# Performance work log

Measured on AMD Instinct MI355X. Metric: run time of the kernel, lower is better.

Reference implementation:

```python
import jax, jax.numpy as jnp
import numpy as np

N_EMBD = 1024
N_HEAD = 16
HEAD_DIM = 64


def setup_inputs() -> dict:
    key = jax.random.key(0)
    ks = jax.random.split(key, 5)
    x = jax.random.normal(ks[0], (4, 2048, N_EMBD), dtype=jnp.float32)
    # qkv_proj: Linear(n_embd, 3*n_embd) -- torch weight is [out, in]
    W_qkv = jax.random.normal(ks[1], (3 * N_EMBD, N_EMBD), dtype=jnp.float32) * 0.02
    b_qkv = jnp.zeros((3 * N_EMBD,), dtype=jnp.float32)
    W_out = jax.random.normal(ks[2], (N_EMBD, N_EMBD), dtype=jnp.float32) * 0.02
    b_out = jnp.zeros((N_EMBD,), dtype=jnp.float32)
    return {"x": x, "W_qkv": W_qkv, "b_qkv": b_qkv, "W_out": W_out, "b_out": b_out}


def reference(x, W_qkv, b_qkv, W_out, b_out):
    B, S, C = x.shape
    scale = 1.0 / np.sqrt(HEAD_DIM)
    qkv = jnp.einsum('bsc,oc->bso', x, W_qkv) + b_qkv  # [B,S,3C]
    q, k, v = jnp.split(qkv, 3, axis=-1)
    # [B,S,C] -> [B,H,S,Dh]
    def to_heads(t):
        return t.reshape(B, S, N_HEAD, HEAD_DIM).transpose(0, 2, 1, 3)
    q, k, v = to_heads(q), to_heads(k), to_heads(v)
    scores = jnp.einsum('bhqd,bhkd->bhqk', q, k) * scale  # [B,H,S,S]
    causal = jnp.tril(jnp.ones((S, S), dtype=bool))
    scores = jnp.where(causal[None, None], scores, -jnp.inf)
    weights = jax.nn.softmax(scores.astype(jnp.float32), axis=-1).astype(q.dtype)
    y = jnp.einsum('bhqk,bhkd->bhqd', weights, v)  # [B,H,S,Dh]
    y = y.transpose(0, 2, 1, 3).reshape(B, S, C)
    return jnp.einsum('bsc,oc->bso', y, W_out) + b_out
```

## Files before the change

### kernel.cpp

```cpp
#include <hip/hip_runtime.h>
#include <stdint.h>
#include <stddef.h>

typedef __attribute__((ext_vector_type(8))) short short8;
typedef __attribute__((ext_vector_type(4))) float f32x4;
typedef __attribute__((ext_vector_type(16))) float f32x16;
typedef __attribute__((ext_vector_type(4))) unsigned short ushort4v;

#define SEQ   2048
#define NH    16
#define BATCH 4
#define GK    1024

__device__ __forceinline__ unsigned short f2bf(float f) {
  union { float f; unsigned int u; } v; v.f = f;
  unsigned int u = v.u;
  u += 0x7fffu + ((u >> 16) & 1u);
  return (unsigned short)(u >> 16);
}

__global__ void cvt_bf16(const float* __restrict__ src, unsigned short* __restrict__ dst, int n4) {
  int i = blockIdx.x * blockDim.x + threadIdx.x;
  const int stride = gridDim.x * blockDim.x;
  for (; i < n4; i += stride) {
    const float4 v = reinterpret_cast<const float4*>(src)[i];
    ushort4v o;
    o[0] = f2bf(v.x); o[1] = f2bf(v.y); o[2] = f2bf(v.z); o[3] = f2bf(v.w);
    reinterpret_cast<ushort4v*>(dst)[i] = o;
  }
}

template<int MODE>
__global__ __launch_bounds__(256, 2)
void gemm_bt(const unsigned short* __restrict__ A,
             const unsigned short* __restrict__ Bw,
             const float* __restrict__ bias,
             unsigned short* __restrict__ q_ws,
             unsigned short* __restrict__ k_ws,
             unsigned short* __restrict__ vt_ws,
             float* __restrict__ fout,
             int N)
{
  __shared__ __attribute__((aligned(16))) unsigned short As[128 * 64];
  __shared__ __attribute__((aligned(16))) unsigned short Bs[128 * 64];

  const int t = threadIdx.x;
  const int w = t >> 6, lane = t & 63;
  const int g = lane >> 4, c = lane & 15;
  const int wrow = w >> 1, wcol = w & 1;
  const int m0 = blockIdx.y * 128;
  const int n0 = blockIdx.x * 128;

  const f32x4 fz = {0.f, 0.f, 0.f, 0.f};
  f32x4 acc[4][4];
#pragma unroll
  for (int i = 0; i < 4; ++i)
#pragma unroll
    for (int j = 0; j < 4; ++j) acc[i][j] = fz;

  int s_row[4], s_cg[4], s_off[4];
#pragma unroll
  for (int i = 0; i < 4; ++i) {
    const int u = (i * 4 + w) * 64 + lane;
    s_row[i] = u >> 3;
    s_cg[i]  = u & 7;
    s_off[i] = s_row[i] * 64 + ((s_cg[i] ^ (s_row[i] & 7)) << 3);
  }

  short8 ra[4], rb[4];
#pragma unroll
  for (int i = 0; i < 4; ++i) {
    ra[i] = *reinterpret_cast<const short8*>(A  + (size_t)(m0 + s_row[i]) * GK + s_cg[i] * 8);
    rb[i] = *reinterpret_cast<const short8*>(Bw + (size_t)(n0 + s_row[i]) * GK + s_cg[i] * 8);
  }

  for (int ks = 0; ks < GK; ks += 64) {
#pragma unroll
    for (int i = 0; i < 4; ++i) {
      *reinterpret_cast<short8*>(&As[s_off[i]]) = ra[i];
      *reinterpret_cast<short8*>(&Bs[s_off[i]]) = rb[i];
    }
    __syncthreads();
    const bool more = (ks + 64) < GK;
    if (more) {
#pragma unroll
      for (int i = 0; i < 4; ++i) {
        ra[i] = *reinterpret_cast<const short8*>(A  + (size_t)(m0 + s_row[i]) * GK + (ks + 64) + s_cg[i] * 8);
        rb[i] = *reinterpret_cast<const short8*>(Bw + (size_t)(n0 + s_row[i]) * GK + (ks + 64) + s_cg[i] * 8);
      }
    }
#pragma unroll
    for (int kk = 0; kk < 2; ++kk) {
      short8 af[4], bfr[4];
#pragma unroll
      for (int mi = 0; mi < 4; ++mi) {
        const int row = wrow * 64 + mi * 16 + c;
        af[mi] = *reinterpret_cast<const short8*>(&As[row * 64 + (((kk * 4 + g) ^ (row & 7)) << 3)]);
      }
#pragma unroll
      for (int ni = 0; ni < 4; ++ni) {
        const int row = wcol * 64 + ni * 16 + c;
        bfr[ni] = *reinterpret_cast<const short8*>(&Bs[row * 64 + (((kk * 4 + g) ^ (row & 7)) << 3)]);
      }
#pragma unroll
      for (int mi = 0; mi < 4; ++mi)
#pragma unroll
        for (int ni = 0; ni < 4; ++ni)
          acc[mi][ni] = __builtin_amdgcn_mfma_f32_16x16x32_bf16(af[mi], bfr[ni], acc[mi][ni], 0, 0, 0);
    }
    __syncthreads();
  }

  if (MODE == 0) {
    const int sec = n0 >> 10;
    if (sec == 2) {
#pragma unroll
      for (int ni = 0; ni < 4; ++ni) {
        const int n = n0 + wcol * 64 + ni * 16 + c;
        const float bb = bias[n];
        const int hh = (n & 1023) >> 6;
        const int d = n & 63;
#pragma unroll
        for (int mi = 0; mi < 4; ++mi) {
#pragma unroll
          for (int r = 0; r < 4; ++r) {
            const int m = m0 + wrow * 64 + mi * 16 + g * 4 + r;
            const int b = m >> 11, s = m & 2047;
            vt_ws[((size_t)((b * NH + hh) * 64 + d)) * SEQ + s] = f2bf(acc[mi][ni][r] + bb);
          }
        }
      }
    } else {
      unsigned short* dst = (sec == 0) ? q_ws : k_ws;
      const float qsc = (sec == 0) ? (0.125f * 1.44269504f) : 1.0f;
#pragma unroll
      for (int ni = 0; ni < 4; ++ni) {
        const int n = n0 + wcol * 64 + ni * 16 + c;
        const float bb = bias[n];
        const int hh = (n & 1023) >> 6;
        const int d = n & 63;
#pragma unroll
        for (int mi = 0; mi < 4; ++mi) {
#pragma unroll
          for (int r = 0; r < 4; ++r) {
            const int m = m0 + wrow * 64 + mi * 16 + g * 4 + r;
            const int b = m >> 11, s = m & 2047;
            const float val = (acc[mi][ni][r] + bb) * qsc;
            dst[((size_t)((b * NH + hh) * SEQ + s) << 6) + d] = f2bf(val);
          }
        }
      }
    }
  } else {
#pragma unroll
    for (int ni = 0; ni < 4; ++ni) {
      const int n = n0 + wcol * 64 + ni * 16 + c;
      const float bb = bias[n];
#pragma unroll
      for (int mi = 0; mi < 4; ++mi) {
#pragma unroll
        for (int r = 0; r < 4; ++r) {
          const int m = m0 + wrow * 64 + mi * 16 + g * 4 + r;
          fout[(size_t)m * N + n] = acc[mi][ni][r] + bb;
        }
      }
    }
  }
}

__global__ __launch_bounds__(256, 2)
void attn_fwd2(const unsigned short* __restrict__ q_ws,
               const unsigned short* __restrict__ k_ws,
               const unsigned short* __restrict__ vt_ws,
               unsigned short* __restrict__ y_ws)
{
  __shared__ __attribute__((aligned(16))) unsigned short Ks[2][64 * 64];
  __shared__ __attribute__((aligned(16))) unsigned short Vs[2][64 * 64];
  __shared__ __attribute__((aligned(16))) unsigned short Pl[4][32 * 64];

  const int t = threadIdx.x;
  const int w = t >> 6, lane = t & 63;
  const int ql = lane & 31;
  const int hi = lane >> 5;
  const int bh = blockIdx.y;
  const int b = bh >> 4, h = bh & 15;

  const int s_row = t >> 3, s_cg = t & 7;
  const int s_off0 = s_row * 64 + ((s_cg ^ (s_row & 7)) << 3);
  const int s_off1 = (s_row + 32) * 64 + ((s_cg ^ (s_row & 7)) << 3);

  unsigned short* Pw = &Pl[w][0];

  short8 rk0, rk1, rv0, rv1;
  const unsigned short* kbase = k_ws + (size_t)bh * SEQ * 64;
  const unsigned short* vbase = vt_ws + (size_t)bh * 64 * SEQ;

  auto stage_issue = [&](int kt) {
    const unsigned short* kp = kbase + (size_t)kt * 64 * 64;
    rk0 = *reinterpret_cast<const short8*>(kp + (size_t)s_row * 64 + s_cg * 8);
    rk1 = *reinterpret_cast<const short8*>(kp + (size_t)(s_row + 32) * 64 + s_cg * 8);
    const unsigned short* vp = vbase + (size_t)kt * 64;
    rv0 = *reinterpret_cast<const short8*>(vp + (size_t)s_row * SEQ + s_cg * 8);
    rv1 = *reinterpret_cast<const short8*>(vp + (size_t)(s_row + 32) * SEQ + s_cg * 8);
  };
  auto stage_write = [&](int bi) {
    *reinterpret_cast<short8*>(&Ks[bi][s_off0]) = rk0;
    *reinterpret_cast<short8*>(&Ks[bi][s_off1]) = rk1;
    *reinterpret_cast<short8*>(&Vs[bi][s_off0]) = rv0;
    *reinterpret_cast<short8*>(&Vs[bi][s_off1]) = rv1;
  };

#pragma unroll 1
  for (int pi = 0; pi < 2; ++pi) {
    const int jt = pi ? (15 - blockIdx.x) : blockIdx.x;
    const int q0 = jt * 128;
    const int wq0 = q0 + w * 32;
    const int nkt = 2 * jt + 2;

    const unsigned short* qrow = q_ws + ((size_t)bh * SEQ + (wq0 + ql)) * 64;
    short8 qf[4];
#pragma unroll
    for (int ks = 0; ks < 4; ++ks)
      qf[ks] = *reinterpret_cast<const short8*>(qrow + ks * 16 + hi * 8);

    f32x16 o0, o1;
#pragma unroll
    for (int i = 0; i < 16; ++i) { o0[i] = 0.f; o1[i] = 0.f; }
    float m_run = -1e30f, lsum = 0.f;

    stage_issue(0);
    stage_write(0);

#pragma unroll 1
    for (int kt = 0; kt < nkt; ++kt) {
      const bool more = (kt + 1) < nkt;
      if (more) stage_issue(kt + 1);
      __syncthreads();
      const int cur = kt & 1;
      const int kt64 = kt * 64;

      if (kt64 <= wq0 + 31) {
        f32x16 sc0, sc1;
#pragma unroll
        for (int i = 0; i < 16; ++i) { sc0[i] = 0.f; sc1[i] = 0.f; }
#pragma unroll
        for (int ks = 0; ks < 4; ++ks) {
          const int r0 = ql, r1 = 32 + ql;
          const short8 kf0 = *reinterpret_cast<const short8*>(
              &Ks[cur][r0 * 64 + (((2 * ks + hi) ^ (r0 & 7)) << 3)]);
          const short8 kf1 = *reinterpret_cast<const short8*>(
              &Ks[cur][r1 * 64 + (((2 * ks + hi) ^ (r1 & 7)) << 3)]);
          sc0 = __builtin_amdgcn_mfma_f32_32x32x16_bf16(kf0, qf[ks], sc0, 0, 0, 0);
          sc1 = __builtin_amdgcn_mfma_f32_32x32x16_bf16(kf1, qf[ks], sc1, 0, 0, 0);
        }
        if (kt64 + 63 > wq0) {
          const int gq = wq0 + ql;
#pragma unroll
          for (int r = 0; r < 16; ++r) {
            const int krow = (r & 3) + 8 * (r >> 2) + 4 * hi;
            if (kt64 + krow > gq)      sc0[r] = -1e30f;
            if (kt64 + 32 + krow > gq) sc1[r] = -1e30f;
          }
        }
        float tm = -1e30f;
#pragma unroll
        for (int r = 0; r < 16; ++r) tm = fmaxf(tm, fmaxf(sc0[r], sc1[r]));
        tm = fmaxf(tm, __shfl_xor(tm, 32));
        if (__any(tm > m_run + 10.0f)) {
          const float m_new = fmaxf(m_run, tm);
          const float al = __builtin_amdgcn_exp2f(m_run - m_new);
          m_run = m_new;
          lsum *= al;
#pragma unroll
          for (int r = 0; r < 16; ++r) {
            const int qq = (r & 3) + 8 * (r >> 2) + 4 * hi;
            const float ar = __shfl(al, qq);
            o0[r] *= ar; o1[r] *= ar;
          }
        }
        float psum = 0.f;
#pragma unroll
        for (int t2 = 0; t2 < 2; ++t2) {
#pragma unroll
          for (int gr = 0; gr < 4; ++gr) {
            const float s0 = (t2 ? sc1[gr * 4 + 0] : sc0[gr * 4 + 0]) - m_run;
            const float s1 = (t2 ? sc1[gr * 4 + 1] : sc0[gr * 4 + 1]) - m_run;
            const float s2 = (t2 ? sc1[gr * 4 + 2] : sc0[gr * 4 + 2]) - m_run;
            const float s3 = (t2 ? sc1[gr * 4 + 3] : sc0[gr * 4 + 3]) - m_run;
            const float p0 = __builtin_amdgcn_exp2f(s0);
            const float p1 = __builtin_amdgcn_exp2f(s1);
            const float p2 = __builtin_amdgcn_exp2f(s2);
            const float p3 = __builtin_amdgcn_exp2f(s3);
            psum += (p0 + p1) + (p2 + p3);
            uint2 pv;
            pv.x = (unsigned)f2bf(p0) | ((unsigned)f2bf(p1) << 16);
            pv.y = (unsigned)f2bf(p2) | ((unsigned)f2bf(p3) << 16);
            const int off = ql * 64 + (((gr + 4 * t2) ^ (ql & 7)) << 3) + 4 * hi;
            *reinterpret_cast<uint2*>(&Pw[off]) = pv;
          }
        }
        lsum += psum;
        short8 pa[4];
#pragma unroll
        for (int ks = 0; ks < 4; ++ks)
          pa[ks] = *reinterpret_cast<const short8*>(
              &Pw[ql * 64 + (((2 * ks + hi) ^ (ql & 7)) << 3)]);
#pragma unroll
        for (int ks = 0; ks < 4; ++ks) {
          const int r0 = ql, r1 = 32 + ql;
          const short8 vf0 = *reinterpret_cast<const short8*>(
              &Vs[cur][r0 * 64 + (((2 * ks + hi) ^ (r0 & 7)) << 3)]);
          const short8 vf1 = *reinterpret_cast<const short8*>(
              &Vs[cur][r1 * 64 + (((2 * ks + hi) ^ (r1 & 7)) << 3)]);
          o0 = __builtin_amdgcn_mfma_f32_32x32x16_bf16(pa[ks], vf0, o0, 0, 0, 0);
          o1 = __builtin_amdgcn_mfma_f32_32x32x16_bf16(pa[ks], vf1, o1, 0, 0, 0);
        }
      }
      if (more) stage_write((kt + 1) & 1);
    }

    lsum += __shfl_xor(lsum, 32);
    const float linv = 1.f / lsum;
#pragma unroll
    for (int r = 0; r < 16; ++r) {
      const int qq = (r & 3) + 8 * (r >> 2) + 4 * hi;
      const float lr = __shfl(linv, qq);
      const size_t rowo = ((size_t)b * SEQ + (wq0 + qq)) * 1024 + h * 64;
      y_ws[rowo + ql]      = f2bf(o0[r] * lr);
      y_ws[rowo + 32 + ql] = f2bf(o1[r] * lr);
    }
    __syncthreads();
  }
}

extern "C" void kernel_launch(void* const* d_in, const int* in_sizes, int n_in,
                              void* d_out, int out_size, void* d_ws, size_t ws_size,
                              hipStream_t stream)
{
  (void)in_sizes; (void)n_in; (void)out_size; (void)ws_size;
  const float* x     = (const float*)d_in[0];
  const float* W_qkv = (const float*)d_in[1];
  const float* b_qkv = (const float*)d_in[2];
  const float* W_out = (const float*)d_in[3];
  const float* b_out = (const float*)d_in[4];
  float* out = (float*)d_out;

  unsigned short* ws      = (unsigned short*)d_ws;
  unsigned short* x_bf    = ws;
  unsigned short* wqkv_bf = x_bf    + (size_t)8192 * 1024;
  unsigned short* wout_bf = wqkv_bf + (size_t)3072 * 1024;
  unsigned short* q_ws    = wout_bf + (size_t)1024 * 1024;
  unsigned short* k_ws    = q_ws    + (size_t)64 * SEQ * 64;
  unsigned short* vt_ws   = k_ws    + (size_t)64 * SEQ * 64;
  unsigned short* y_ws    = vt_ws   + (size_t)64 * SEQ * 64;

  cvt_bf16<<<2048, 256, 0, stream>>>(x,     x_bf,    (8192 * 1024) / 4);
  cvt_bf16<<<1024, 256, 0, stream>>>(W_qkv, wqkv_bf, (3072 * 1024) / 4);
  cvt_bf16<<<512,  256, 0, stream>>>(W_out, wout_bf, (1024 * 1024) / 4);

  gemm_bt<0><<<dim3(24, 64), 256, 0, stream>>>(x_bf, wqkv_bf, b_qkv, q_ws, k_ws, vt_ws, nullptr, 3072);
  attn_fwd2<<<dim3(8, 64), 256, 0, stream>>>(q_ws, k_ws, vt_ws, y_ws);
  gemm_bt<1><<<dim3(8, 64), 256, 0, stream>>>(y_ws, wout_bf, b_out, nullptr, nullptr, nullptr, out, 1024);
}
```

Measured before the change: 185.0 us.

## Rework GEMM loads to direct-to-LDS, separate V transpose, larger attention query tiles

The GEMM now stages A/B tiles through global_load_lds directly into shared memory instead of register prefetch, dropping the software double-buffering. The V output of the QKV GEMM is written row-major and then transposed by a separate kernel, replacing the strided scattered stores. The attention kernel now processes 64 query rows per wave (two 32-row subtiles sharing K/V fragments). P is packed into MFMA operands in registers via cvt_pk_bf16 and permlane32 swaps instead of round-tripping through LDS. This trades an extra kernel launch and the loss of GEMM prefetch overlap for better K/V reuse and less LDS traffic. It also halves the attention grid, which may reduce occupancy.

```diff
diff --git a/kernel.cpp b/kernel.cpp
--- a/kernel.cpp
+++ b/kernel.cpp
@@ -6,6 +6,7 @@
 typedef __attribute__((ext_vector_type(4))) float f32x4;
 typedef __attribute__((ext_vector_type(16))) float f32x16;
 typedef __attribute__((ext_vector_type(4))) unsigned short ushort4v;
+typedef __attribute__((ext_vector_type(4))) unsigned int uint4v;
 
 #define SEQ   2048
 #define NH    16
@@ -17,6 +18,32 @@
   unsigned int u = v.u;
   u += 0x7fffu + ((u >> 16) & 1u);
   return (unsigned short)(u >> 16);
+}
+
+__device__ __forceinline__ unsigned cvtpk_bf16(float lo, float hi) {
+  unsigned r;
+  asm("v_cvt_pk_bf16_f32 %0, %1, %2" : "=v"(r) : "v"(lo), "v"(hi));
+  return r;
+}
+
+__device__ __forceinline__ void plswap(unsigned &x, unsigned &y) {
+#if __has_builtin(__builtin_amdgcn_permlane32_swap)
+  auto r = __builtin_amdgcn_permlane32_swap((int)x, (int)y, false, false);
+  x = (unsigned)r[0]; y = (unsigned)r[1];
+#else
+  const unsigned sx = (unsigned)__shfl_xor((int)x, 32);
+  const unsigned sy = (unsigned)__shfl_xor((int)y, 32);
+  const bool hi = (threadIdx.x & 63) >= 32;
+  const unsigned nx = hi ? sy : x;
+  const unsigned ny = hi ? y : sx;
+  x = nx; y = ny;
+#endif
+}
+
+__device__ __forceinline__ void gload16(const unsigned short* g, unsigned short* l) {
+  __builtin_amdgcn_global_load_lds(
+      (const __attribute__((address_space(1))) unsigned int*)g,
+      (__attribute__((address_space(3))) unsigned int*)l, 16, 0, 0);
 }
 
 __global__ void cvt_bf16(const float* __restrict__ src, unsigned short* __restrict__ dst, int n4) {
@@ -37,7 +64,7 @@
              const float* __restrict__ bias,
              unsigned short* __restrict__ q_ws,
              unsigned short* __restrict__ k_ws,
-             unsigned short* __restrict__ vt_ws,
+             unsigned short* __restrict__ v_ws,
              float* __restrict__ fout,
              int N)
 {
@@ -51,6 +78,9 @@
   const int m0 = blockIdx.y * 128;
   const int n0 = blockIdx.x * 128;
 
+  const int r8 = lane >> 3;
+  const int cgs = (lane & 7) ^ r8;
+
   const f32x4 fz = {0.f, 0.f, 0.f, 0.f};
   f32x4 acc[4][4];
 #pragma unroll
@@ -58,37 +88,15 @@
 #pragma unroll
     for (int j = 0; j < 4; ++j) acc[i][j] = fz;
 
-  int s_row[4], s_cg[4], s_off[4];
-#pragma unroll
-  for (int i = 0; i < 4; ++i) {
-    const int u = (i * 4 + w) * 64 + lane;
-    s_row[i] = u >> 3;
-    s_cg[i]  = u & 7;
-    s_off[i] = s_row[i] * 64 + ((s_cg[i] ^ (s_row[i] & 7)) << 3);
-  }
-
-  short8 ra[4], rb[4];
-#pragma unroll
-  for (int i = 0; i < 4; ++i) {
-    ra[i] = *reinterpret_cast<const short8*>(A  + (size_t)(m0 + s_row[i]) * GK + s_cg[i] * 8);
-    rb[i] = *reinterpret_cast<const short8*>(Bw + (size_t)(n0 + s_row[i]) * GK + s_cg[i] * 8);
-  }
-
   for (int ks = 0; ks < GK; ks += 64) {
+    __syncthreads();
 #pragma unroll
     for (int i = 0; i < 4; ++i) {
-      *reinterpret_cast<short8*>(&As[s_off[i]]) = ra[i];
-      *reinterpret_cast<short8*>(&Bs[s_off[i]]) = rb[i];
+      const int RB = (i * 4 + w) * 8;
+      gload16(A + (size_t)(m0 + RB + r8) * GK + ks + cgs * 8, &As[RB * 64]);
+      gload16(Bw + (size_t)(n0 + RB + r8) * GK + ks + cgs * 8, &Bs[RB * 64]);
     }
     __syncthreads();
-    const bool more = (ks + 64) < GK;
-    if (more) {
-#pragma unroll
-      for (int i = 0; i < 4; ++i) {
-        ra[i] = *reinterpret_cast<const short8*>(A  + (size_t)(m0 + s_row[i]) * GK + (ks + 64) + s_cg[i] * 8);
-        rb[i] = *reinterpret_cast<const short8*>(Bw + (size_t)(n0 + s_row[i]) * GK + (ks + 64) + s_cg[i] * 8);
-      }
-    }
 #pragma unroll
     for (int kk = 0; kk < 2; ++kk) {
       short8 af[4], bfr[4];
@@ -108,54 +116,34 @@
         for (int ni = 0; ni < 4; ++ni)
           acc[mi][ni] = __builtin_amdgcn_mfma_f32_16x16x32_bf16(af[mi], bfr[ni], acc[mi][ni], 0, 0, 0);
     }
-    __syncthreads();
   }
 
   if (MODE == 0) {
     const int sec = n0 >> 10;
-    if (sec == 2) {
-#pragma unroll
-      for (int ni = 0; ni < 4; ++ni) {
-        const int n = n0 + wcol * 64 + ni * 16 + c;
-        const float bb = bias[n];
-        const int hh = (n & 1023) >> 6;
-        const int d = n & 63;
-#pragma unroll
-        for (int mi = 0; mi < 4; ++mi) {
-#pragma unroll
-          for (int r = 0; r < 4; ++r) {
-            const int m = m0 + wrow * 64 + mi * 16 + g * 4 + r;
-            const int b = m >> 11, s = m & 2047;
-            vt_ws[((size_t)((b * NH + hh) * 64 + d)) * SEQ + s] = f2bf(acc[mi][ni][r] + bb);
-          }
-        }
-      }
-    } else {
-      unsigned short* dst = (sec == 0) ? q_ws : k_ws;
-      const float qsc = (sec == 0) ? (0.125f * 1.44269504f) : 1.0f;
-#pragma unroll
-      for (int ni = 0; ni < 4; ++ni) {
-        const int n = n0 + wcol * 64 + ni * 16 + c;
-        const float bb = bias[n];
-        const int hh = (n & 1023) >> 6;
-        const int d = n & 63;
-#pragma unroll
-        for (int mi = 0; mi < 4; ++mi) {
-#pragma unroll
-          for (int r = 0; r < 4; ++r) {
-            const int m = m0 + wrow * 64 + mi * 16 + g * 4 + r;
-            const int b = m >> 11, s = m & 2047;
-            const float val = (acc[mi][ni][r] + bb) * qsc;
-            dst[((size_t)((b * NH + hh) * SEQ + s) << 6) + d] = f2bf(val);
-          }
-        }
-      }
-    }
-  } else {
+    unsigned short* dst = (sec == 0) ? q_ws : ((sec == 1) ? k_ws : v_ws);
+    const float qsc = (sec == 0) ? (0.125f * 1.44269504f) : 1.0f;
 #pragma unroll
     for (int ni = 0; ni < 4; ++ni) {
       const int n = n0 + wcol * 64 + ni * 16 + c;
       const float bb = bias[n];
+      const int hh = (n & 1023) >> 6;
+      const int d = n & 63;
+#pragma unroll
+      for (int mi = 0; mi < 4; ++mi) {
+#pragma unroll
+        for (int r = 0; r < 4; ++r) {
+          const int m = m0 + wrow * 64 + mi * 16 + g * 4 + r;
+          const int b = m >> 11, s = m & 2047;
+          const float val = (acc[mi][ni][r] + bb) * qsc;
+          dst[((size_t)((b * NH + hh) * SEQ + s) << 6) + d] = f2bf(val);
+        }
+      }
+    }
+  } else {
+#pragma unroll
+    for (int ni = 0; ni < 4; ++ni) {
+      const int n = n0 + wcol * 64 + ni * 16 + c;
+      const float bb = bias[n];
 #pragma unroll
       for (int mi = 0; mi < 4; ++mi) {
 #pragma unroll
@@ -168,68 +156,140 @@
   }
 }
 
+__global__ __launch_bounds__(256)
+void transpose_v(const unsigned short* __restrict__ v, unsigned short* __restrict__ vt) {
+  __shared__ unsigned short T[64][72];
+  const int t = threadIdx.x;
+  const int bh = blockIdx.y, s0 = blockIdx.x * 64;
+  const unsigned short* src = v + ((size_t)bh * SEQ + s0) * 64;
+#pragma unroll
+  for (int rep = 0; rep < 2; ++rep) {
+    const int u = rep * 256 + t;
+    const int sr = u >> 3, cg = u & 7;
+    const short8 x = *reinterpret_cast<const short8*>(src + (size_t)sr * 64 + cg * 8);
+    *reinterpret_cast<short8*>(&T[sr][cg * 8]) = x;
+  }
+  __syncthreads();
+  unsigned short* dst = vt + (size_t)bh * 64 * SEQ + s0;
+#pragma unroll
+  for (int rep = 0; rep < 2; ++rep) {
+    const int u = rep * 256 + t;
+    const int d = u >> 3, sc8 = u & 7;
+    short8 x;
+#pragma unroll
+    for (int j = 0; j < 8; ++j) x[j] = (short)T[sc8 * 8 + j][d];
+    *reinterpret_cast<short8*>(dst + (size_t)d * SEQ + sc8 * 8) = x;
+  }
+}
+
 __global__ __launch_bounds__(256, 2)
-void attn_fwd2(const unsigned short* __restrict__ q_ws,
+void attn_fwd3(const unsigned short* __restrict__ q_ws,
                const unsigned short* __restrict__ k_ws,
                const unsigned short* __restrict__ vt_ws,
                unsigned short* __restrict__ y_ws)
 {
   __shared__ __attribute__((aligned(16))) unsigned short Ks[2][64 * 64];
   __shared__ __attribute__((aligned(16))) unsigned short Vs[2][64 * 64];
-  __shared__ __attribute__((aligned(16))) unsigned short Pl[4][32 * 64];
 
   const int t = threadIdx.x;
   const int w = t >> 6, lane = t & 63;
-  const int ql = lane & 31;
-  const int hi = lane >> 5;
-  const int bh = blockIdx.y;
-  const int b = bh >> 4, h = bh & 15;
+  const int ql = lane & 31, hi = lane >> 5;
+  const int bh = blockIdx.y, b = bh >> 4, h = bh & 15;
 
   const int s_row = t >> 3, s_cg = t & 7;
-  const int s_off0 = s_row * 64 + ((s_cg ^ (s_row & 7)) << 3);
-  const int s_off1 = (s_row + 32) * 64 + ((s_cg ^ (s_row & 7)) << 3);
-
-  unsigned short* Pw = &Pl[w][0];
-
-  short8 rk0, rk1, rv0, rv1;
+  const int so0 = s_row * 64 + ((s_cg ^ (s_row & 7)) << 3);
+  const int so1 = (s_row + 32) * 64 + ((s_cg ^ (s_row & 7)) << 3);
+
   const unsigned short* kbase = k_ws + (size_t)bh * SEQ * 64;
   const unsigned short* vbase = vt_ws + (size_t)bh * 64 * SEQ;
 
+  short8 rk0, rk1, rv0, rv1;
   auto stage_issue = [&](int kt) {
     const unsigned short* kp = kbase + (size_t)kt * 64 * 64;
     rk0 = *reinterpret_cast<const short8*>(kp + (size_t)s_row * 64 + s_cg * 8);
     rk1 = *reinterpret_cast<const short8*>(kp + (size_t)(s_row + 32) * 64 + s_cg * 8);
-    const unsigned short* vp = vbase + (size_t)kt * 64;
+    const unsigned short* vp = vbase + kt * 64;
     rv0 = *reinterpret_cast<const short8*>(vp + (size_t)s_row * SEQ + s_cg * 8);
     rv1 = *reinterpret_cast<const short8*>(vp + (size_t)(s_row + 32) * SEQ + s_cg * 8);
   };
   auto stage_write = [&](int bi) {
-    *reinterpret_cast<short8*>(&Ks[bi][s_off0]) = rk0;
-    *reinterpret_cast<short8*>(&Ks[bi][s_off1]) = rk1;
-    *reinterpret_cast<short8*>(&Vs[bi][s_off0]) = rv0;
-    *reinterpret_cast<short8*>(&Vs[bi][s_off1]) = rv1;
+    *reinterpret_cast<short8*>(&Ks[bi][so0]) = rk0;
+    *reinterpret_cast<short8*>(&Ks[bi][so1]) = rk1;
+    *reinterpret_cast<short8*>(&Vs[bi][so0]) = rv0;
+    *reinterpret_cast<short8*>(&Vs[bi][so1]) = rv1;
   };
 
 #pragma unroll 1
   for (int pi = 0; pi < 2; ++pi) {
-    const int jt = pi ? (15 - blockIdx.x) : blockIdx.x;
-    const int q0 = jt * 128;
-    const int wq0 = q0 + w * 32;
-    const int nkt = 2 * jt + 2;
-
-    const unsigned short* qrow = q_ws + ((size_t)bh * SEQ + (wq0 + ql)) * 64;
-    short8 qf[4];
-#pragma unroll
-    for (int ks = 0; ks < 4; ++ks)
-      qf[ks] = *reinterpret_cast<const short8*>(qrow + ks * 16 + hi * 8);
-
-    f32x16 o0, o1;
-#pragma unroll
-    for (int i = 0; i < 16; ++i) { o0[i] = 0.f; o1[i] = 0.f; }
-    float m_run = -1e30f, lsum = 0.f;
+    const int jt = pi ? (7 - blockIdx.x) : blockIdx.x;
+    const int wq0 = jt * 256 + w * 64;
+    const int nkt = 4 * jt + 4;
+
+    const unsigned short* qrA = q_ws + ((size_t)bh * SEQ + (wq0 + ql)) * 64;
+    const unsigned short* qrB = qrA + 32 * 64;
+    short8 qfA[4], qfB[4];
+#pragma unroll
+    for (int ks = 0; ks < 4; ++ks) {
+      qfA[ks] = *reinterpret_cast<const short8*>(qrA + ks * 16 + hi * 8);
+      qfB[ks] = *reinterpret_cast<const short8*>(qrB + ks * 16 + hi * 8);
+    }
+
+    f32x16 oA0, oA1, oB0, oB1;
+#pragma unroll
+    for (int i = 0; i < 16; ++i) { oA0[i] = 0.f; oA1[i] = 0.f; oB0[i] = 0.f; oB1[i] = 0.f; }
+    float mA = -1e30f, lA = 0.f, mB = -1e30f, lB = 0.f;
 
     stage_issue(0);
     stage_write(0);
+
+    auto softmax_pack = [&](f32x16& s0, f32x16& s1, float& m_run, float& lsum,
+                            f32x16& o0, f32x16& o1, short8* pa) {
+      float tm = -1e30f;
+#pragma unroll
+      for (int r = 0; r < 16; ++r) tm = fmaxf(tm, fmaxf(s0[r], s1[r]));
+      tm = fmaxf(tm, __shfl_xor(tm, 32));
+      if (__any(tm > m_run + 10.0f)) {
+        const float m_new = fmaxf(m_run, tm);
+        const float al = __builtin_amdgcn_exp2f(m_run - m_new);
+        m_run = m_new;
+        lsum *= al;
+#pragma unroll
+        for (int r = 0; r < 16; ++r) {
+          const int qq = (r & 3) + 8 * (r >> 2) + 4 * hi;
+          const float ar = __shfl(al, qq);
+          o0[r] *= ar; o1[r] *= ar;
+        }
+      }
+      float psum = 0.f;
+      unsigned W[16];
+#pragma unroll
+      for (int half = 0; half < 2; ++half) {
+#pragma unroll
+        for (int gr = 0; gr < 4; ++gr) {
+          const float v0 = (half ? s1[gr * 4 + 0] : s0[gr * 4 + 0]) - m_run;
+          const float v1 = (half ? s1[gr * 4 + 1] : s0[gr * 4 + 1]) - m_run;
+          const float v2 = (half ? s1[gr * 4 + 2] : s0[gr * 4 + 2]) - m_run;
+          const float v3 = (half ? s1[gr * 4 + 3] : s0[gr * 4 + 3]) - m_run;
+          const float p0 = __builtin_amdgcn_exp2f(v0);
+          const float p1 = __builtin_amdgcn_exp2f(v1);
+          const float p2 = __builtin_amdgcn_exp2f(v2);
+          const float p3 = __builtin_amdgcn_exp2f(v3);
+          psum += (p0 + p1) + (p2 + p3);
+          W[half * 8 + 2 * gr]     = cvtpk_bf16(p0, p1);
+          W[half * 8 + 2 * gr + 1] = cvtpk_bf16(p2, p3);
+        }
+      }
+      lsum += psum;
+#pragma unroll
+      for (int q4 = 0; q4 < 4; ++q4) {
+        unsigned a0 = W[q4 * 4 + 0], a1 = W[q4 * 4 + 2];
+        unsigned b0 = W[q4 * 4 + 1], b1 = W[q4 * 4 + 3];
+        plswap(a0, a1);
+        plswap(b0, b1);
+        uint4v pk; pk[0] = a0; pk[1] = b0; pk[2] = a1; pk[3] = b1;
+        pa[q4] = __builtin_bit_cast(short8, pk);
+      }
+    };
 
 #pragma unroll 1
     for (int kt = 0; kt < nkt; ++kt) {
@@ -239,96 +299,89 @@
       const int cur = kt & 1;
       const int kt64 = kt * 64;
 
-      if (kt64 <= wq0 + 31) {
-        f32x16 sc0, sc1;
-#pragma unroll
-        for (int i = 0; i < 16; ++i) { sc0[i] = 0.f; sc1[i] = 0.f; }
+      if (kt64 <= wq0 + 63) {
+        short8 kfl[4], kfh[4];
 #pragma unroll
         for (int ks = 0; ks < 4; ++ks) {
-          const int r0 = ql, r1 = 32 + ql;
-          const short8 kf0 = *reinterpret_cast<const short8*>(
-              &Ks[cur][r0 * 64 + (((2 * ks + hi) ^ (r0 & 7)) << 3)]);
-          const short8 kf1 = *reinterpret_cast<const short8*>(
-              &Ks[cur][r1 * 64 + (((2 * ks + hi) ^ (r1 & 7)) << 3)]);
-          sc0 = __builtin_amdgcn_mfma_f32_32x32x16_bf16(kf0, qf[ks], sc0, 0, 0, 0);
-          sc1 = __builtin_amdgcn_mfma_f32_32x32x16_bf16(kf1, qf[ks], sc1, 0, 0, 0);
-        }
-        if (kt64 + 63 > wq0) {
-          const int gq = wq0 + ql;
-#pragma unroll
-          for (int r = 0; r < 16; ++r) {
-            const int krow = (r & 3) + 8 * (r >> 2) + 4 * hi;
-            if (kt64 + krow > gq)      sc0[r] = -1e30f;
-            if (kt64 + 32 + krow > gq) sc1[r] = -1e30f;
+          kfl[ks] = *reinterpret_cast<const short8*>(
+              &Ks[cur][ql * 64 + (((2 * ks + hi) ^ (ql & 7)) << 3)]);
+          kfh[ks] = *reinterpret_cast<const short8*>(
+              &Ks[cur][(32 + ql) * 64 + (((2 * ks + hi) ^ (ql & 7)) << 3)]);
+        }
+        const bool actA = kt64 <= wq0 + 31;
+        short8 paA[4], paB[4];
+
+        if (actA) {
+          f32x16 s0, s1;
+#pragma unroll
+          for (int i = 0; i < 16; ++i) { s0[i] = 0.f; s1[i] = 0.f; }
+#pragma unroll
+          for (int ks = 0; ks < 4; ++ks) {
+            s0 = __builtin_amdgcn_mfma_f32_32x32x16_bf16(kfl[ks], qfA[ks], s0, 0, 0, 0);
+            s1 = __builtin_amdgcn_mfma_f32_32x32x16_bf16(kfh[ks], qfA[ks], s1, 0, 0, 0);
           }
-        }
-        float tm = -1e30f;
-#pragma unroll
-        for (int r = 0; r < 16; ++r) tm = fmaxf(tm, fmaxf(sc0[r], sc1[r]));
-        tm = fmaxf(tm, __shfl_xor(tm, 32));
-        if (__any(tm > m_run + 10.0f)) {
-          const float m_new = fmaxf(m_run, tm);
-          const float al = __builtin_amdgcn_exp2f(m_run - m_new);
-          m_run = m_new;
-          lsum *= al;
-#pragma unroll
-          for (int r = 0; r < 16; ++r) {
-            const int qq = (r & 3) + 8 * (r >> 2) + 4 * hi;
-            const float ar = __shfl(al, qq);
-            o0[r] *= ar; o1[r] *= ar;
+          if (kt64 + 63 > wq0) {
+            const int gq = wq0 + ql;
+#pragma unroll
+            for (int r = 0; r < 16; ++r) {
+              const int krow = (r & 3) + 8 * (r >> 2) + 4 * hi;
+              if (kt64 + krow > gq)      s0[r] = -1e30f;
+              if (kt64 + 32 + krow > gq) s1[r] = -1e30f;
+            }
           }
-        }
-        float psum = 0.f;
-#pragma unroll
-        for (int t2 = 0; t2 < 2; ++t2) {
-#pragma unroll
-          for (int gr = 0; gr < 4; ++gr) {
-            const float s0 = (t2 ? sc1[gr * 4 + 0] : sc0[gr * 4 + 0]) - m_run;
-            const float s1 = (t2 ? sc1[gr * 4 + 1] : sc0[gr * 4 + 1]) - m_run;
-            const float s2 = (t2 ? sc1[gr * 4 + 2] : sc0[gr * 4 + 2]) - m_run;
-            const float s3 = (t2 ? sc1[gr * 4 + 3] : sc0[gr * 4 + 3]) - m_run;
-            const float p0 = __builtin_amdgcn_exp2f(s0);
-            const float p1 = __builtin_amdgcn_exp2f(s1);
-            const float p2 = __builtin_amdgcn_exp2f(s2);
-            const float p3 = __builtin_amdgcn_exp2f(s3);
-            psum += (p0 + p1) + (p2 + p3);
-            uint2 pv;
-            pv.x = (unsigned)f2bf(p0) | ((unsigned)f2bf(p1) << 16);
-            pv.y = (unsigned)f2bf(p2) | ((unsigned)f2bf(p3) << 16);
-            const int off = ql * 64 + (((gr + 4 * t2) ^ (ql & 7)) << 3) + 4 * hi;
-            *reinterpret_cast<uint2*>(&Pw[off]) = pv;
+          softmax_pack(s0, s1, mA, lA, oA0, oA1, paA);
+        }
+        {
+          f32x16 s0, s1;
+#pragma unroll
+          for (int i = 0; i < 16; ++i) { s0[i] = 0.f; s1[i] = 0.f; }
+#pragma unroll
+          for (int ks = 0; ks < 4; ++ks) {
+            s0 = __builtin_amdgcn_mfma_f32_32x32x16_bf16(kfl[ks], qfB[ks], s0, 0, 0, 0);
+            s1 = __builtin_amdgcn_mfma_f32_32x32x16_bf16(kfh[ks], qfB[ks], s1, 0, 0, 0);
           }
-        }
-        lsum += psum;
-        short8 pa[4];
-#pragma unroll
-        for (int ks = 0; ks < 4; ++ks)
-          pa[ks] = *reinterpret_cast<const short8*>(
-              &Pw[ql * 64 + (((2 * ks + hi) ^ (ql & 7)) << 3)]);
+          if (kt64 + 63 > wq0 + 32) {
+            const int gq = wq0 + 32 + ql;
+#pragma unroll
+            for (int r = 0; r < 16; ++r) {
+              const int krow = (r & 3) + 8 * (r >> 2) + 4 * hi;
+              if (kt64 + krow > gq)      s0[r] = -1e30f;
+              if (kt64 + 32 + krow > gq) s1[r] = -1e30f;
+            }
+          }
+          softmax_pack(s0, s1, mB, lB, oB0, oB1, paB);
+        }
 #pragma unroll
         for (int ks = 0; ks < 4; ++ks) {
-          const int r0 = ql, r1 = 32 + ql;
-          const short8 vf0 = *reinterpret_cast<const short8*>(
-              &Vs[cur][r0 * 64 + (((2 * ks + hi) ^ (r0 & 7)) << 3)]);
-          const short8 vf1 = *reinterpret_cast<const short8*>(
-              &Vs[cur][r1 * 64 + (((2 * ks + hi) ^ (r1 & 7)) << 3)]);
-          o0 = __builtin_amdgcn_mfma_f32_32x32x16_bf16(pa[ks], vf0, o0, 0, 0, 0);
-          o1 = __builtin_amdgcn_mfma_f32_32x32x16_bf16(pa[ks], vf1, o1, 0, 0, 0);
+          const short8 vfl = *reinterpret_cast<const short8*>(
+              &Vs[cur][ql * 64 + (((2 * ks + hi) ^ (ql & 7)) << 3)]);
+          const short8 vfh = *reinterpret_cast<const short8*>(
+              &Vs[cur][(32 + ql) * 64 + (((2 * ks + hi) ^ (ql & 7)) << 3)]);
+          oB0 = __builtin_amdgcn_mfma_f32_32x32x16_bf16(paB[ks], vfl, oB0, 0, 0, 0);
+          oB1 = __builtin_amdgcn_mfma_f32_32x32x16_bf16(paB[ks], vfh, oB1, 0, 0, 0);
+          if (actA) {
+            oA0 = __builtin_amdgcn_mfma_f32_32x32x16_bf16(paA[ks], vfl, oA0, 0, 0, 0);
+            oA1 = __builtin_amdgcn_mfma_f32_32x32x16_bf16(paA[ks], vfh, oA1, 0, 0, 0);
+          }
         }
       }
       if (more) stage_write((kt + 1) & 1);
     }
 
-    lsum += __shfl_xor(lsum, 32);
-    const float linv = 1.f / lsum;
-#pragma unroll
-    for (int r = 0; r < 16; ++r) {
-      const int qq = (r & 3) + 8 * (r >> 2) + 4 * hi;
-      const float lr = __shfl(linv, qq);
-      const size_t rowo = ((size_t)b * SEQ + (wq0 + qq)) * 1024 + h * 64;
-      y_ws[rowo + ql]      = f2bf(o0[r] * lr);
-      y_ws[rowo + 32 + ql] = f2bf(o1[r] * lr);
-    }
+    auto fin = [&](f32x16& o0, f32x16& o1, float lsum, int qbase) {
+      lsum += __shfl_xor(lsum, 32);
+      const float linv = 1.f / lsum;
+#pragma unroll
+      for (int r = 0; r < 16; ++r) {
+        const int qq = (r & 3) + 8 * (r >> 2) + 4 * hi;
+        const float lr = __shfl(linv, qq);
+        const size_t rowo = ((size_t)b * SEQ + (qbase + qq)) * 1024 + h * 64;
+        y_ws[rowo + ql]      = f2bf(o0[r] * lr);
+        y_ws[rowo + 32 + ql] = f2bf(o1[r] * lr);
+      }
+    };
+    fin(oA0, oA1, lA, wq0);
+    fin(oB0, oB1, lB, wq0 + 32);
     __syncthreads();
   }
 }
@@ -351,14 +404,16 @@
   unsigned short* wout_bf = wqkv_bf + (size_t)3072 * 1024;
   unsigned short* q_ws    = wout_bf + (size_t)1024 * 1024;
   unsigned short* k_ws    = q_ws    + (size_t)64 * SEQ * 64;
-  unsigned short* vt_ws   = k_ws    + (size_t)64 * SEQ * 64;
-  unsigned short* y_ws    = vt_ws   + (size_t)64 * SEQ * 64;
+  unsigned short* v_ws    = k_ws    + (size_t)64 * SEQ * 64;
+  unsigned short* y_ws    = v_ws    + (size_t)64 * SEQ * 64;
+  unsigned short* vt_ws   = x_bf;
 
   cvt_bf16<<<2048, 256, 0, stream>>>(x,     x_bf,    (8192 * 1024) / 4);
   cvt_bf16<<<1024, 256, 0, stream>>>(W_qkv, wqkv_bf, (3072 * 1024) / 4);
   cvt_bf16<<<512,  256, 0, stream>>>(W_out, wout_bf, (1024 * 1024) / 4);
 
-  gemm_bt<0><<<dim3(24, 64), 256, 0, stream>>>(x_bf, wqkv_bf, b_qkv, q_ws, k_ws, vt_ws, nullptr, 3072);
-  attn_fwd2<<<dim3(8, 64), 256, 0, stream>>>(q_ws, k_ws, vt_ws, y_ws);
+  gemm_bt<0><<<dim3(24, 64), 256, 0, stream>>>(x_bf, wqkv_bf, b_qkv, q_ws, k_ws, v_ws, nullptr, 3072);
+  transpose_v<<<dim3(SEQ / 64, 64), 256, 0, stream>>>(v_ws, vt_ws);
+  attn_fwd3<<<dim3(4, 64), 256, 0, stream>>>(q_ws, k_ws, vt_ws, y_ws);
   gemm_bt<1><<<dim3(8, 64), 256, 0, stream>>>(y_ws, wout_bf, b_out, nullptr, nullptr, nullptr, out, 1024);
 }
```

After: 193.6 us. 4.6% more time.
